# Kernel optimization log

Hardware: AMD Instinct MI355X
Metric: run time of the kernel (lower is better)

## Reference

```python
import jax, jax.numpy as jnp
import numpy as np

F_SIZE = 256
GF_REDUCE = 0x1D  # low byte of galois' default primitive polynomial 0x11D for GF(2^8)


def _gf256_mul_table() -> np.ndarray:
    """Full 256x256 GF(2^8) multiplication table (poly x^8+x^4+x^3+x^2+1 = 0x11D),
    matching galois.GF(2**8) multiplication, built by Russian-peasant multiply."""
    a = np.broadcast_to(np.arange(F_SIZE, dtype=np.uint16)[:, None], (F_SIZE, F_SIZE)).copy()
    b = np.broadcast_to(np.arange(F_SIZE, dtype=np.uint16)[None, :], (F_SIZE, F_SIZE)).copy()
    res = np.zeros((F_SIZE, F_SIZE), dtype=np.uint16)
    for _ in range(8):
        res ^= np.where(b & 1, a, 0).astype(np.uint16)
        b >>= 1
        hi = a & 0x80
        a = (a << 1) & 0xFF
        a ^= np.where(hi, GF_REDUCE, 0).astype(np.uint16)
    return res.astype(np.int32)


def _xor_reduce_last(x: jnp.ndarray) -> jnp.ndarray:
    # associative tree XOR-fold over the last axis (replaces the python for-loop fold)
    return jax.lax.reduce(x, np.int32(0), jax.lax.bitwise_xor, (x.ndim - 1,))


def setup_inputs() -> dict:
    key = jax.random.key(0)
    k_m, k_s, k_P = jax.random.split(key, 3)
    B, K, N = 32, 16, 256
    m = jax.random.randint(k_m, (B, K), 0, F_SIZE, dtype=jnp.int32)
    s = jax.random.randint(k_s, (B, N), 0, F_SIZE, dtype=jnp.int32)
    P = jax.random.randint(k_P, (K, N, N), 0, F_SIZE, dtype=jnp.int32)
    table = jnp.asarray(_gf256_mul_table())  # [256,256] int32
    return {"m": m, "s": s, "P": P, "table": table}


def reference(m, s, P, table):
    # m: [B,K] int32, s: [B,N] int32, P: [K,N,N] int32, table: [256,256] int32
    # s_times_P[b,i,j] = XOR_l  s[b,l] * P[i,j,l]   (GF(256) mat-vec per check i)
    prod1 = table[s[:, None, None, :], P[None, :, :, :]]          # [B,K,N,N]
    s_times_P = _xor_reduce_last(prod1)                            # [B,K,N]
    # m_check[b,i] = (XOR_j  s_times_P[b,i,j] * s[b,j]) - m[b,i]  i.e. s^T P_i s - m
    prod2 = table[s_times_P, s[:, None, :]]                        # [B,K,N]
    m_check = _xor_reduce_last(prod2) - m                          # [B,K]
    return jnp.maximum(1 - m_check.sum(-1), 0)                     # relu(1 - sum) -> [B]
```

## Files before the change

kernel.cpp:

```cpp
#include <hip/hip_runtime.h>
#include <stdint.h>

enum { B_ = 32, K_ = 16, N_ = 256 };

#define WS_NEED 2048

#define M4 0x01010101u

__device__ __forceinline__ uint32_t pack4i(int4 v) {
    return (uint32_t)(v.x & 255) | ((uint32_t)(v.y & 255) << 8) |
           ((uint32_t)(v.z & 255) << 16) | ((uint32_t)(v.w & 255) << 24);
}

__global__ __launch_bounds__(512) void gf_main5(const int* __restrict__ s32,
                                                const int* __restrict__ P32,
                                                int* __restrict__ part) {
    __shared__ uint32_t ptile[256 * 64];
    __shared__ __align__(16) uint8_t cvb[2][2048];
    __shared__ uint32_t wr[8];

    const int k = blockIdx.x & 15, bp = blockIdx.x >> 4;
    const int tid = threadIdx.x;
    const int bb = __builtin_amdgcn_readfirstlane(tid >> 8);
    const int j = tid & 255;

    uint32_t c = (uint32_t)s32[(bp * 2 + bb) * 256 + j] & 255u;
    uint32_t A = 0, Bw = 0;
#pragma unroll
    for (int u = 0; u < 4; ++u) {
        A |= c << (8 * u);
        c = ((c << 1) & 255u) ^ ((c >> 7) * 29u);
    }
#pragma unroll
    for (int u = 0; u < 4; ++u) {
        Bw |= c << (8 * u);
        c = ((c << 1) & 255u) ^ ((c >> 7) * 29u);
    }
    uint32_t by[8];
#pragma unroll
    for (int r = 0; r < 8; ++r) {
        uint32_t t = (A >> r) & M4;
        uint32_t lo = (t | (t >> 7) | (t >> 14) | (t >> 21)) & 15u;
        uint32_t u2 = (Bw >> r) & M4;
        uint32_t hi = (u2 | (u2 >> 7) | (u2 >> 14) | (u2 >> 21)) & 15u;
        by[r] = lo | (hi << 4);
        cvb[bb][r * 256 + j] = (uint8_t)by[r];
    }
    const uint32_t ct0 = by[0] | (by[1] << 8) | (by[2] << 16) | (by[3] << 24);
    const uint32_t ct1 = by[4] | (by[5] << 8) | (by[6] << 16) | (by[7] << 24);

    const int4* praw = (const int4*)P32 + (size_t)k * 16384;
#pragma unroll 8
    for (int it = 0; it < 32; ++it) {
        const int g = tid + 512 * it;
        uint32_t w = pack4i(praw[g]);
        const int n = g >> 6, ihi = (g >> 2) & 15, wq = g & 3;
        ptile[(n << 6) + (((ihi ^ (n & 15))) << 2) + wq] = w;
    }
    __syncthreads();

    const int n = j;
    const uint4* cv4 = (const uint4*)cvb[bb];
    const uint32_t* prow = &ptile[n << 6];
    const int nx = n & 15;
    uint32_t xr0 = 0, xr1 = 0, xr2 = 0, xr3 = 0, xr4 = 0, xr5 = 0, xr6 = 0, xr7 = 0;
#pragma unroll 4
    for (int i = 0; i < 16; ++i) {
        uint4 p = *(const uint4*)(prow + ((i ^ nx) << 2));
#define CACC(xr, r)                                                        \
        {                                                                  \
            uint4 cc = cv4[r * 16 + i];                                    \
            xr ^= (cc.x & p.x) ^ (cc.y & p.y) ^ (cc.z & p.z) ^ (cc.w & p.w); \
        }
        CACC(xr0, 0) CACC(xr1, 1) CACC(xr2, 2) CACC(xr3, 3)
        CACC(xr4, 4) CACC(xr5, 5) CACC(xr6, 6) CACC(xr7, 7)
#undef CACC
    }
    uint32_t stP = (uint32_t)(__popc(xr0) & 1) | ((uint32_t)(__popc(xr1) & 1) << 1) |
                   ((uint32_t)(__popc(xr2) & 1) << 2) | ((uint32_t)(__popc(xr3) & 1) << 3) |
                   ((uint32_t)(__popc(xr4) & 1) << 4) | ((uint32_t)(__popc(xr5) & 1) << 5) |
                   ((uint32_t)(__popc(xr6) & 1) << 6) | ((uint32_t)(__popc(xr7) & 1) << 7);

    uint32_t prod = 0;
#pragma unroll
    for (int r = 0; r < 4; ++r)
        prod |= (uint32_t)(__popc(stP & ((ct0 >> (8 * r)) & 255u)) & 1) << r;
#pragma unroll
    for (int r = 0; r < 4; ++r)
        prod |= (uint32_t)(__popc(stP & ((ct1 >> (8 * r)) & 255u)) & 1) << (r + 4);

    uint32_t acc = prod;
#pragma unroll
    for (int off = 1; off < 64; off <<= 1) acc ^= __shfl_xor(acc, off, 64);
    if ((tid & 63) == 0) wr[tid >> 6] = acc;
    __syncthreads();
    if (tid == 0) {
        int p0 = (int)(wr[0] ^ wr[1] ^ wr[2] ^ wr[3]);
        int p1 = (int)(wr[4] ^ wr[5] ^ wr[6] ^ wr[7]);
        part[(bp * 2 + 0) * 16 + k] = p0;
        part[(bp * 2 + 1) * 16 + k] = p1;
    }
}

__global__ __launch_bounds__(512) void gf_fin(const int* __restrict__ part,
                                              const int* __restrict__ m32,
                                              int* __restrict__ dout) {
    __shared__ int sd[512];
    const int t = threadIdx.x;
    sd[t] = part[t] - m32[t];
    __syncthreads();
    if (t < 32) {
        int s = 0;
#pragma unroll
        for (int kk = 0; kk < 16; ++kk) s += sd[t * 16 + kk];
        dout[t] = max(1 - s, 0);
    }
}

__global__ void prep_zero(int* __restrict__ out) {
    if (threadIdx.x < B_) out[threadIdx.x] = 0;
}
#define LK(sw, pw)                                                  \
    v ^= tbl[(((sw) & 255u) << 8) | ((pw) & 255u)];                 \
    v ^= tbl[((sw) & 0xFF00u) | (((pw) >> 8) & 255u)];              \
    v ^= tbl[(((sw) >> 8) & 0xFF00u) | (((pw) >> 16) & 255u)];      \
    v ^= tbl[(((sw) >> 16) & 0xFF00u) | ((pw) >> 24)];
__global__ __launch_bounds__(256) void gf_main_fb(const int* __restrict__ m,
                                                  const int* __restrict__ s32,
                                                  const int* __restrict__ P32,
                                                  const int* __restrict__ t32,
                                                  int* __restrict__ out) {
    __shared__ uint8_t tbl[65536];
    __shared__ uint8_t sb[256];
    __shared__ uint32_t wred[4];
    const int b = blockIdx.x >> 4, k = blockIdx.x & 15, tid = threadIdx.x;
    for (int i = tid; i < 16384; i += 256) {
        int4 v = ((const int4*)t32)[i];
        ((uint32_t*)tbl)[i] = pack4i(v);
    }
    if (tid < 64) {
        int4 v = ((const int4*)s32)[b * 64 + tid];
        ((uint32_t*)sb)[tid] = pack4i(v);
    }
    __syncthreads();
    uint32_t v = 0;
    const uint32_t* sw32 = (const uint32_t*)sb;
    const int4* prow32 = (const int4*)(P32 + ((size_t)k * N_ + tid) * N_);
#pragma unroll 4
    for (int j0 = 0; j0 < 64; j0 += 4) {
        uint32_t p0 = pack4i(prow32[j0]), p1 = pack4i(prow32[j0 + 1]);
        uint32_t p2 = pack4i(prow32[j0 + 2]), p3 = pack4i(prow32[j0 + 3]);
        uint32_t w0 = sw32[j0], w1 = sw32[j0 + 1], w2 = sw32[j0 + 2], w3 = sw32[j0 + 3];
        LK(w0, p0) LK(w1, p1) LK(w2, p2) LK(w3, p3)
    }
    uint32_t wv = tbl[(v << 8) | (uint32_t)sb[tid]];
#pragma unroll
    for (int off = 1; off < 64; off <<= 1) wv ^= __shfl_xor(wv, off, 64);
    if ((tid & 63) == 0) wred[tid >> 6] = wv;
    __syncthreads();
    if (tid == 0) {
        uint32_t x = wred[0] ^ wred[1] ^ wred[2] ^ wred[3];
        atomicAdd(&out[b], (int)x - m[b * K_ + k]);
    }
}
__global__ void gf_finish_fb(int* __restrict__ out) {
    if (threadIdx.x < B_) {
        int v = out[threadIdx.x];
        out[threadIdx.x] = max(1 - v, 0);
    }
}

extern "C" void kernel_launch(void* const* d_in, const int* in_sizes, int n_in,
                              void* d_out, int out_size, void* d_ws, size_t ws_size,
                              hipStream_t stream) {
    const int* m     = (const int*)d_in[0];
    const int* s     = (const int*)d_in[1];
    const int* P     = (const int*)d_in[2];
    const int* table = (const int*)d_in[3];
    int* out = (int*)d_out;

    if (ws_size >= (size_t)WS_NEED) {
        int* part = (int*)d_ws;
        gf_main5<<<256, 512, 0, stream>>>(s, P, part);
        gf_fin<<<1, 512, 0, stream>>>(part, m, out);
    } else {
        prep_zero<<<1, 64, 0, stream>>>(out);
        gf_main_fb<<<B_ * K_, 256, 0, stream>>>(m, s, P, table, out);
        gf_finish_fb<<<1, 64, 0, stream>>>(out);
    }
}
```

Before: 15.47 us.

## Split P rows across block pairs and process four batches per block

Each block now loads half of a check matrix P_k (128 rows) and handles four batch vectors instead of two, so every P tile in LDS serves twice as many batches and per-block global traffic is halved. The inner loop is split over the i-dimension between wave halves, and each thread accumulates two rows. Partial parities are exchanged through LDS, and the per-row-half results are written separately and XOR-combined in the finishing kernel. This adds an extra LDS exchange, a barrier, and a larger partials buffer, in exchange for better reuse of each P load.

```diff
diff --git a/kernel.cpp b/kernel.cpp
--- a/kernel.cpp
+++ b/kernel.cpp
@@ -3,7 +3,7 @@
 
 enum { B_ = 32, K_ = 16, N_ = 256 };
 
-#define WS_NEED 2048
+#define WS_NEED 4096
 
 #define M4 0x01010101u
 
@@ -12,93 +12,126 @@
            ((uint32_t)(v.z & 255) << 16) | ((uint32_t)(v.w & 255) << 24);
 }
 
-__global__ __launch_bounds__(512) void gf_main5(const int* __restrict__ s32,
+__global__ __launch_bounds__(512) void gf_main6(const int* __restrict__ s32,
                                                 const int* __restrict__ P32,
                                                 int* __restrict__ part) {
-    __shared__ uint32_t ptile[256 * 64];
-    __shared__ __align__(16) uint8_t cvb[2][2048];
+    __shared__ uint32_t ptile[128 * 64];
+    __shared__ __align__(16) uint8_t cvb[4][2048];
+    __shared__ uint2 ct_lds[4][256];
+    __shared__ uint32_t xch[4][2][128];
     __shared__ uint32_t wr[8];
 
-    const int k = blockIdx.x & 15, bp = blockIdx.x >> 4;
+    const int bid = blockIdx.x;
+    const int k = bid & 15, nh = (bid >> 4) & 1, bq = bid >> 5;
     const int tid = threadIdx.x;
-    const int bb = __builtin_amdgcn_readfirstlane(tid >> 8);
-    const int j = tid & 255;
-
-    uint32_t c = (uint32_t)s32[(bp * 2 + bb) * 256 + j] & 255u;
-    uint32_t A = 0, Bw = 0;
-#pragma unroll
-    for (int u = 0; u < 4; ++u) {
-        A |= c << (8 * u);
-        c = ((c << 1) & 255u) ^ ((c >> 7) * 29u);
-    }
-#pragma unroll
-    for (int u = 0; u < 4; ++u) {
-        Bw |= c << (8 * u);
-        c = ((c << 1) & 255u) ^ ((c >> 7) * 29u);
-    }
-    uint32_t by[8];
-#pragma unroll
-    for (int r = 0; r < 8; ++r) {
-        uint32_t t = (A >> r) & M4;
-        uint32_t lo = (t | (t >> 7) | (t >> 14) | (t >> 21)) & 15u;
-        uint32_t u2 = (Bw >> r) & M4;
-        uint32_t hi = (u2 | (u2 >> 7) | (u2 >> 14) | (u2 >> 21)) & 15u;
-        by[r] = lo | (hi << 4);
-        cvb[bb][r * 256 + j] = (uint8_t)by[r];
-    }
-    const uint32_t ct0 = by[0] | (by[1] << 8) | (by[2] << 16) | (by[3] << 24);
-    const uint32_t ct1 = by[4] | (by[5] << 8) | (by[6] << 16) | (by[7] << 24);
-
-    const int4* praw = (const int4*)P32 + (size_t)k * 16384;
+
+    {
+        const int j = tid & 255;
+#pragma unroll
+        for (int e = 0; e < 2; ++e) {
+            const int bbx = (tid >> 8) + 2 * e;
+            uint32_t c = (uint32_t)s32[(bq * 4 + bbx) * 256 + j] & 255u;
+            uint32_t A = 0, Bw = 0;
+#pragma unroll
+            for (int u = 0; u < 4; ++u) {
+                A |= c << (8 * u);
+                c = ((c << 1) & 255u) ^ ((c >> 7) * 29u);
+            }
+#pragma unroll
+            for (int u = 0; u < 4; ++u) {
+                Bw |= c << (8 * u);
+                c = ((c << 1) & 255u) ^ ((c >> 7) * 29u);
+            }
+            uint32_t by[8];
+#pragma unroll
+            for (int r = 0; r < 8; ++r) {
+                uint32_t t = (A >> r) & M4;
+                uint32_t lo = (t | (t >> 7) | (t >> 14) | (t >> 21)) & 15u;
+                uint32_t u2 = (Bw >> r) & M4;
+                uint32_t hi = (u2 | (u2 >> 7) | (u2 >> 14) | (u2 >> 21)) & 15u;
+                by[r] = lo | (hi << 4);
+                cvb[bbx][r * 256 + j] = (uint8_t)by[r];
+            }
+            uint2 ct;
+            ct.x = by[0] | (by[1] << 8) | (by[2] << 16) | (by[3] << 24);
+            ct.y = by[4] | (by[5] << 8) | (by[6] << 16) | (by[7] << 24);
+            ct_lds[bbx][j] = ct;
+        }
+    }
+
+    const int4* praw = (const int4*)P32 + (size_t)k * 16384 + nh * 8192;
 #pragma unroll 8
-    for (int it = 0; it < 32; ++it) {
+    for (int it = 0; it < 16; ++it) {
         const int g = tid + 512 * it;
         uint32_t w = pack4i(praw[g]);
         const int n = g >> 6, ihi = (g >> 2) & 15, wq = g & 3;
-        ptile[(n << 6) + (((ihi ^ (n & 15))) << 2) + wq] = w;
-    }
-    __syncthreads();
-
-    const int n = j;
-    const uint4* cv4 = (const uint4*)cvb[bb];
-    const uint32_t* prow = &ptile[n << 6];
-    const int nx = n & 15;
-    uint32_t xr0 = 0, xr1 = 0, xr2 = 0, xr3 = 0, xr4 = 0, xr5 = 0, xr6 = 0, xr7 = 0;
+        ptile[(n << 6) + ((ihi ^ (n & 15)) << 2) + wq] = w;
+    }
+    __syncthreads();
+
+    {
+        const int bh = __builtin_amdgcn_readfirstlane(tid >> 6);
+        const int bb = bh >> 1, h = bh & 1;
+        const int nl = tid & 63;
+        const int nx = nl & 15;
+        const uint4* cvq = (const uint4*)cvb[bb];
+        const uint32_t* prow0 = &ptile[nl << 6];
+        const uint32_t* prow1 = &ptile[(nl + 64) << 6];
+        uint32_t xa0 = 0, xa1 = 0, xa2 = 0, xa3 = 0, xa4 = 0, xa5 = 0, xa6 = 0, xa7 = 0;
+        uint32_t xb0 = 0, xb1 = 0, xb2 = 0, xb3 = 0, xb4 = 0, xb5 = 0, xb6 = 0, xb7 = 0;
 #pragma unroll 4
-    for (int i = 0; i < 16; ++i) {
-        uint4 p = *(const uint4*)(prow + ((i ^ nx) << 2));
-#define CACC(xr, r)                                                        \
-        {                                                                  \
-            uint4 cc = cv4[r * 16 + i];                                    \
-            xr ^= (cc.x & p.x) ^ (cc.y & p.y) ^ (cc.z & p.z) ^ (cc.w & p.w); \
+        for (int ii = 0; ii < 8; ++ii) {
+            const int i = 8 * h + ii;
+            const int slot = (i ^ nx) << 2;
+            uint4 p0 = *(const uint4*)(prow0 + slot);
+            uint4 p1 = *(const uint4*)(prow1 + slot);
+#define CACC(xa, xb, r)                                                       \
+            {                                                                 \
+                uint4 cc = cvq[(r) * 16 + i];                                 \
+                xa ^= (cc.x & p0.x) ^ (cc.y & p0.y) ^ (cc.z & p0.z) ^ (cc.w & p0.w); \
+                xb ^= (cc.x & p1.x) ^ (cc.y & p1.y) ^ (cc.z & p1.z) ^ (cc.w & p1.w); \
+            }
+            CACC(xa0, xb0, 0) CACC(xa1, xb1, 1) CACC(xa2, xb2, 2) CACC(xa3, xb3, 3)
+            CACC(xa4, xb4, 4) CACC(xa5, xb5, 5) CACC(xa6, xb6, 6) CACC(xa7, xb7, 7)
+#undef CACC
         }
-        CACC(xr0, 0) CACC(xr1, 1) CACC(xr2, 2) CACC(xr3, 3)
-        CACC(xr4, 4) CACC(xr5, 5) CACC(xr6, 6) CACC(xr7, 7)
-#undef CACC
-    }
-    uint32_t stP = (uint32_t)(__popc(xr0) & 1) | ((uint32_t)(__popc(xr1) & 1) << 1) |
-                   ((uint32_t)(__popc(xr2) & 1) << 2) | ((uint32_t)(__popc(xr3) & 1) << 3) |
-                   ((uint32_t)(__popc(xr4) & 1) << 4) | ((uint32_t)(__popc(xr5) & 1) << 5) |
-                   ((uint32_t)(__popc(xr6) & 1) << 6) | ((uint32_t)(__popc(xr7) & 1) << 7);
-
-    uint32_t prod = 0;
-#pragma unroll
-    for (int r = 0; r < 4; ++r)
-        prod |= (uint32_t)(__popc(stP & ((ct0 >> (8 * r)) & 255u)) & 1) << r;
-#pragma unroll
-    for (int r = 0; r < 4; ++r)
-        prod |= (uint32_t)(__popc(stP & ((ct1 >> (8 * r)) & 255u)) & 1) << (r + 4);
-
-    uint32_t acc = prod;
-#pragma unroll
-    for (int off = 1; off < 64; off <<= 1) acc ^= __shfl_xor(acc, off, 64);
-    if ((tid & 63) == 0) wr[tid >> 6] = acc;
+        uint32_t pa = (uint32_t)(__popc(xa0) & 1) | ((uint32_t)(__popc(xa1) & 1) << 1) |
+                      ((uint32_t)(__popc(xa2) & 1) << 2) | ((uint32_t)(__popc(xa3) & 1) << 3) |
+                      ((uint32_t)(__popc(xa4) & 1) << 4) | ((uint32_t)(__popc(xa5) & 1) << 5) |
+                      ((uint32_t)(__popc(xa6) & 1) << 6) | ((uint32_t)(__popc(xa7) & 1) << 7);
+        uint32_t pb = (uint32_t)(__popc(xb0) & 1) | ((uint32_t)(__popc(xb1) & 1) << 1) |
+                      ((uint32_t)(__popc(xb2) & 1) << 2) | ((uint32_t)(__popc(xb3) & 1) << 3) |
+                      ((uint32_t)(__popc(xb4) & 1) << 4) | ((uint32_t)(__popc(xb5) & 1) << 5) |
+                      ((uint32_t)(__popc(xb6) & 1) << 6) | ((uint32_t)(__popc(xb7) & 1) << 7);
+        xch[bb][h][nl] = pa;
+        xch[bb][h][nl + 64] = pb;
+    }
+    __syncthreads();
+
+    {
+        const int bb = tid >> 7, nl = tid & 127;
+        uint32_t stP = xch[bb][0][nl] ^ xch[bb][1][nl];
+        uint2 ct = ct_lds[bb][nh * 128 + nl];
+        uint32_t prod = 0;
+#pragma unroll
+        for (int r = 0; r < 4; ++r)
+            prod |= (uint32_t)(__popc(stP & ((ct.x >> (8 * r)) & 255u)) & 1) << r;
+#pragma unroll
+        for (int r = 0; r < 4; ++r)
+            prod |= (uint32_t)(__popc(stP & ((ct.y >> (8 * r)) & 255u)) & 1) << (r + 4);
+
+        uint32_t acc = prod;
+#pragma unroll
+        for (int off = 1; off < 64; off <<= 1) acc ^= __shfl_xor(acc, off, 64);
+        if ((tid & 63) == 0) wr[tid >> 6] = acc;
+    }
     __syncthreads();
     if (tid == 0) {
-        int p0 = (int)(wr[0] ^ wr[1] ^ wr[2] ^ wr[3]);
-        int p1 = (int)(wr[4] ^ wr[5] ^ wr[6] ^ wr[7]);
-        part[(bp * 2 + 0) * 16 + k] = p0;
-        part[(bp * 2 + 1) * 16 + k] = p1;
+#pragma unroll
+        for (int bb = 0; bb < 4; ++bb) {
+            int pv = (int)(wr[2 * bb] ^ wr[2 * bb + 1]);
+            part[(bq * 4 + bb) * 32 + k * 2 + nh] = pv;
+        }
     }
 }
 
@@ -107,7 +140,7 @@
                                               int* __restrict__ dout) {
     __shared__ int sd[512];
     const int t = threadIdx.x;
-    sd[t] = part[t] - m32[t];
+    sd[t] = (int)(((const uint32_t*)part)[2 * t] ^ ((const uint32_t*)part)[2 * t + 1]) - m32[t];
     __syncthreads();
     if (t < 32) {
         int s = 0;
@@ -181,7 +214,7 @@
 
     if (ws_size >= (size_t)WS_NEED) {
         int* part = (int*)d_ws;
-        gf_main5<<<256, 512, 0, stream>>>(s, P, part);
+        gf_main6<<<256, 512, 0, stream>>>(s, P, part);
         gf_fin<<<1, 512, 0, stream>>>(part, m, out);
     } else {
         prep_zero<<<1, 64, 0, stream>>>(out);
```

After: 13.66 us. 1.13x faster.
